# Kernel tuning notes

Measured on AMD Instinct MI355X. Metric: run time of the kernel, lower is better.

Reference implementation:

```python
import jax, jax.numpy as jnp
import numpy as np

NUM_HEADS = 12


def get_rel_pos(q_size, k_size, rel_pos):
    # rel_pos: (2*max(q,k)-1, head_dim); sizes match table here so no resize.
    max_rel_dist = int(2 * max(q_size, k_size) - 1)
    if rel_pos.shape[0] != max_rel_dist:
        rel_pos = jax.image.resize(rel_pos, (max_rel_dist, rel_pos.shape[1]), method='linear')
    q_coords = jnp.arange(q_size)[:, None] * max(k_size / q_size, 1.0)
    k_coords = jnp.arange(k_size)[None, :] * max(q_size / k_size, 1.0)
    rel = (q_coords - k_coords + (k_size - 1) * max(q_size / k_size, 1.0)).astype(jnp.int32)
    return rel_pos[rel.reshape(-1)].reshape(q_size, k_size, -1)  # (q, k, head_dim)


def setup_inputs() -> dict:
    key = jax.random.key(0)
    ks = jax.random.split(key, 7)
    B, H, W, C = 8, 32, 32, 768
    head_dim = C // NUM_HEADS
    return {
        'x': jax.random.normal(ks[0], (B, H, W, C), jnp.float32),
        'w_qkv': jax.random.normal(ks[1], (C, 3 * C), jnp.float32) * 0.02,
        'b_qkv': jnp.zeros((3 * C,), jnp.float32),
        'rel_pos_h': jax.random.normal(ks[2], (2 * H - 1, head_dim), jnp.float32) * 0.02,
        'rel_pos_w': jax.random.normal(ks[3], (2 * W - 1, head_dim), jnp.float32) * 0.02,
        'w_proj': jax.random.normal(ks[4], (C, C), jnp.float32) * 0.02,
        'b_proj': jnp.zeros((C,), jnp.float32),
    }


def reference(x, w_qkv, b_qkv, rel_pos_h, rel_pos_w, w_proj, b_proj):
    B, H, W, C = x.shape
    heads = NUM_HEADS
    hd = C // heads
    S = H * W
    qkv = x @ w_qkv + b_qkv                                  # (B,H,W,3C)
    qkv = qkv.reshape(B, S, 3, heads, hd).transpose(2, 0, 3, 1, 4)
    qkv = qkv.reshape(3, B * heads, S, hd)
    q, k, v = qkv[0], qkv[1], qkv[2]
    attn = (q * hd ** -0.5) @ k.transpose(0, 2, 1)           # (B*heads, S, S)
    rh = get_rel_pos(H, H, rel_pos_h)                        # (H,H,hd)
    rw = get_rel_pos(W, W, rel_pos_w)                        # (W,W,hd)
    r_q = q.reshape(B * heads, H, W, hd)
    rel_h = jnp.einsum('bhwc,hkc->bhwk', r_q, rh)
    rel_w = jnp.einsum('bhwc,wkc->bhwk', r_q, rw)
    attn = (attn.reshape(B * heads, H, W, H, W)
            + rel_h[:, :, :, :, None]
            + rel_w[:, :, :, None, :]).reshape(B * heads, S, S)
    attn = jax.nn.softmax(attn, axis=-1)
    out = (attn @ v).reshape(B, heads, H, W, hd).transpose(0, 2, 3, 1, 4).reshape(B, H, W, C)
    return out @ w_proj + b_proj
```

## Files before the change

### kernel.cpp

```cpp
#include <hip/hip_runtime.h>
#include <hip/hip_bf16.h>

#define BATCH 8
#define SEQ   1024
#define CH    768
#define NH    12
#define HD    64
#define BH    96
#define N_QKV 2304

#define LOG2E 1.44269504088896f

typedef __attribute__((ext_vector_type(8))) short bfrag;
typedef __attribute__((ext_vector_type(4))) short short4v;
typedef __attribute__((ext_vector_type(4))) float ffrag;

__device__ __forceinline__ short f2bf(float x) {
    __hip_bfloat16 h = __float2bfloat16(x);
    return *reinterpret_cast<short*>(&h);
}
__device__ __forceinline__ float bf2f(short b) {
    __hip_bfloat16 h;
    *reinterpret_cast<short*>(&h) = b;
    return __bfloat162float(h);
}
__device__ __forceinline__ void split2(float x, short& hi, short& lo) {
    short h = f2bf(x);
    hi = h;
    lo = f2bf(x - bf2f(h));
}
__device__ __forceinline__ void async_copy16(void* lds, const void* g) {
    __builtin_amdgcn_global_load_lds(
        (const __attribute__((address_space(1))) void*)g,
        (__attribute__((address_space(3))) void*)lds, 16, 0, 0);
}

__global__ __launch_bounds__(256) void prep(
    const float* __restrict__ x,
    const float* __restrict__ w_qkv, const float* __restrict__ w_proj,
    short* __restrict__ Xh,
    short* __restrict__ WqhT, short* __restrict__ WqlT,
    short* __restrict__ WphT, short* __restrict__ WplT)
{
    __shared__ float ts[32][33];
    const int tid = threadIdx.x;
    const int bid = blockIdx.x;

    if (bid < 512) {
        const int n4 = (BATCH * SEQ * CH) / 4;
        for (int i = bid * 256 + tid; i < n4; i += 512 * 256) {
            float4 f = ((const float4*)x)[i];
            short4v h;
            h[0] = f2bf(f.x); h[1] = f2bf(f.y); h[2] = f2bf(f.z); h[3] = f2bf(f.w);
            ((short4v*)Xh)[i] = h;
        }
        return;
    }
    const float* in; short* hiT; short* loT; int R, C, bx, by;
    if (bid < 2240) {
        int t = bid - 512;  bx = t % 72; by = t / 72;
        in = w_qkv; hiT = WqhT; loT = WqlT; R = CH; C = N_QKV;
    } else {
        int t = bid - 2240; bx = t % 24; by = t / 24;
        in = w_proj; hiT = WphT; loT = WplT; R = CH; C = CH;
    }
    const int r0 = by * 32, c0 = bx * 32;
    #pragma unroll
    for (int i = 0; i < 4; ++i) {
        int idx = tid + i * 256;
        int rr = idx >> 5, cc = idx & 31;
        ts[rr][cc] = in[(size_t)(r0 + rr) * C + c0 + cc];
    }
    __syncthreads();
    #pragma unroll
    for (int i = 0; i < 4; ++i) {
        int idx = tid + i * 256;
        int rr = idx >> 5, cc = idx & 31;
        short h, l;
        split2(ts[cc][rr], h, l);
        hiT[(size_t)(c0 + rr) * R + r0 + cc] = h;
        loT[(size_t)(c0 + rr) * R + r0 + cc] = l;
    }
}

__device__ __forceinline__ void gemm_core2(
    short* lds,
    const short* __restrict__ Ah,
    const short* __restrict__ BhT, const short* __restrict__ BlT,
    int m0, int n0, ffrag acc[4][4])
{
    const int tid = threadIdx.x;
    const int wave = tid >> 6, lane = tid & 63;
    const int quad = lane >> 4, l16 = lane & 15;
    const int wm = (wave & 1) * 64, wn = (wave >> 1) * 64;

    const short* src = Ah;
    int row0 = m0, ldso = 0;
    if (wave == 2)      { src = BhT; row0 = n0; ldso = 8192;  }
    else if (wave == 3) { src = BlT; row0 = n0; ldso = 16384; }
    const size_t lane_off = (size_t)(lane >> 3) * CH + (size_t)((lane & 7) ^ (lane >> 3)) * 8;
    const short* sbase = src + (size_t)row0 * CH + lane_off;
    short* ldsw = lds + ldso;

    for (int c = 0; c < 12; ++c) {
        __syncthreads();
        if (wave != 1) {
            #pragma unroll
            for (int i = 0; i < 16; ++i)
                async_copy16(ldsw + i * 512, sbase + (size_t)i * 8 * CH + c * 64);
        }
        __syncthreads();

        #pragma unroll
        for (int kc = 0; kc < 2; ++kc) {
            bfrag ah[4], bh[4], bl[4];
            const int xs = ((kc * 4 + quad) ^ (l16 & 7)) * 8;
            #pragma unroll
            for (int i = 0; i < 4; ++i) {
                int ra = (wm + i * 16 + l16) * 64 + xs;
                int rb = (wn + i * 16 + l16) * 64 + xs;
                ah[i] = *(const bfrag*)&lds[ra];
                bh[i] = *(const bfrag*)&lds[8192 + rb];
                bl[i] = *(const bfrag*)&lds[16384 + rb];
            }
            #pragma unroll
            for (int mi = 0; mi < 4; ++mi)
                #pragma unroll
                for (int ni = 0; ni < 4; ++ni) {
                    acc[mi][ni] = __builtin_amdgcn_mfma_f32_16x16x32_bf16(ah[mi], bh[ni], acc[mi][ni], 0, 0, 0);
                    acc[mi][ni] = __builtin_amdgcn_mfma_f32_16x16x32_bf16(ah[mi], bl[ni], acc[mi][ni], 0, 0, 0);
                }
        }
    }
}

__device__ __forceinline__ void gemm_core3(
    short* lds,
    const short* __restrict__ Ah, const short* __restrict__ Al,
    const short* __restrict__ BhT, const short* __restrict__ BlT,
    int m0, int n0, ffrag acc[4][4])
{
    const int tid = threadIdx.x;
    const int wave = tid >> 6, lane = tid & 63;
    const int quad = lane >> 4, l16 = lane & 15;
    const int wm = (wave & 1) * 64, wn = (wave >> 1) * 64;

    const short* src;
    int row0;
    if (wave == 0)      { src = Ah;  row0 = m0; }
    else if (wave == 1) { src = Al;  row0 = m0; }
    else if (wave == 2) { src = BhT; row0 = n0; }
    else                { src = BlT; row0 = n0; }
    const size_t lane_off = (size_t)(lane >> 3) * CH + (size_t)((lane & 7) ^ (lane >> 3)) * 8;
    const short* sbase = src + (size_t)row0 * CH + lane_off;
    short* ldsw = lds + wave * 8192;

    for (int c = 0; c < 12; ++c) {
        __syncthreads();
        #pragma unroll
        for (int i = 0; i < 16; ++i)
            async_copy16(ldsw + i * 512, sbase + (size_t)i * 8 * CH + c * 64);
        __syncthreads();

        #pragma unroll
        for (int kc = 0; kc < 2; ++kc) {
            bfrag ah[4], al[4], bh[4], bl[4];
            const int xs = ((kc * 4 + quad) ^ (l16 & 7)) * 8;
            #pragma unroll
            for (int i = 0; i < 4; ++i) {
                int ra = (wm + i * 16 + l16) * 64 + xs;
                int rb = (wn + i * 16 + l16) * 64 + xs;
                ah[i] = *(const bfrag*)&lds[ra];
                al[i] = *(const bfrag*)&lds[8192 + ra];
                bh[i] = *(const bfrag*)&lds[16384 + rb];
                bl[i] = *(const bfrag*)&lds[24576 + rb];
            }
            #pragma unroll
            for (int mi = 0; mi < 4; ++mi)
                #pragma unroll
                for (int ni = 0; ni < 4; ++ni) {
                    acc[mi][ni] = __builtin_amdgcn_mfma_f32_16x16x32_bf16(ah[mi], bh[ni], acc[mi][ni], 0, 0, 0);
                    acc[mi][ni] = __builtin_amdgcn_mfma_f32_16x16x32_bf16(ah[mi], bl[ni], acc[mi][ni], 0, 0, 0);
                    acc[mi][ni] = __builtin_amdgcn_mfma_f32_16x16x32_bf16(al[mi], bh[ni], acc[mi][ni], 0, 0, 0);
                }
        }
    }
}

__global__ __launch_bounds__(256) void gemm_qkv_mfma(
    const short* __restrict__ Xh,
    const short* __restrict__ WhT, const short* __restrict__ WlT,
    const float* __restrict__ bias,
    short* __restrict__ qh, short* __restrict__ kh, short* __restrict__ vT)
{
    __shared__ short lds[3 * 8192];
    const int id  = blockIdx.x;
    const int xcd = id & 7;
    const int per = id >> 3;
    const int m0 = (xcd * 8 + per / 18) * 128;
    const int n0 = (per % 18) * 128;
    const int which = n0 / CH;

    ffrag acc[4][4];
    #pragma unroll
    for (int i = 0; i < 4; ++i)
        #pragma unroll
        for (int j = 0; j < 4; ++j) acc[i][j] = (ffrag){0.f, 0.f, 0.f, 0.f};

    gemm_core2(lds, Xh, WhT, WlT, m0, n0, acc);

    const int tid = threadIdx.x;
    const int wave = tid >> 6, lane = tid & 63;
    const int quad = lane >> 4, l16 = lane & 15;
    const int wm = (wave & 1) * 64, wn = (wave >> 1) * 64;
    const int b = m0 >> 10;

    #pragma unroll
    for (int ni = 0; ni < 4; ++ni) {
        int n = n0 + wn + ni * 16 + l16;
        float bv = bias[n];
        int nin = n - which * CH;
        int head = nin >> 6, d = nin & 63;
        #pragma unroll
        for (int mi = 0; mi < 4; ++mi) {
            if (which == 2) {
                int s_base = (m0 & 1023) + wm + mi * 16 + quad * 4;
                short4v pk;
                #pragma unroll
                for (int r = 0; r < 4; ++r) pk[r] = f2bf(acc[mi][ni][r] + bv);
                *(short4v*)&vT[((size_t)(b * NH + head) * HD + d) * SEQ + s_base] = pk;
            } else {
                const float scale = (which == 0) ? 0.125f * LOG2E : 1.0f;
                short* dst = (which == 0) ? qh : kh;
                #pragma unroll
                for (int r = 0; r < 4; ++r) {
                    int m = m0 + wm + mi * 16 + quad * 4 + r;
                    int s = m & 1023;
                    dst[((size_t)(b * NH + head) * SEQ + s) * HD + d] =
                        f2bf((acc[mi][ni][r] + bv) * scale);
                }
            }
        }
    }
}

__global__ __launch_bounds__(256) void gemm_proj_mfma(
    const short* __restrict__ Ah, const short* __restrict__ Al,
    const short* __restrict__ WhT, const short* __restrict__ WlT,
    const float* __restrict__ bias, float* __restrict__ out)
{
    __shared__ short lds[4 * 8192];
    const int id  = blockIdx.x;
    const int xcd = id & 7;
    const int per = id >> 3;
    const int m0 = (xcd * 8 + per / 6) * 128;
    const int n0 = (per % 6) * 128;

    ffrag acc[4][4];
    #pragma unroll
    for (int i = 0; i < 4; ++i)
        #pragma unroll
        for (int j = 0; j < 4; ++j) acc[i][j] = (ffrag){0.f, 0.f, 0.f, 0.f};

    gemm_core3(lds, Ah, Al, WhT, WlT, m0, n0, acc);

    const int tid = threadIdx.x;
    const int wave = tid >> 6, lane = tid & 63;
    const int quad = lane >> 4, l16 = lane & 15;
    const int wm = (wave & 1) * 64, wn = (wave >> 1) * 64;

    #pragma unroll
    for (int ni = 0; ni < 4; ++ni) {
        int n = n0 + wn + ni * 16 + l16;
        float bv = bias[n];
        #pragma unroll
        for (int mi = 0; mi < 4; ++mi)
            #pragma unroll
            for (int r = 0; r < 4; ++r) {
                int m = m0 + wm + mi * 16 + quad * 4 + r;
                out[(size_t)m * CH + n] = acc[mi][ni][r] + bv;
            }
    }
}

__global__ __launch_bounds__(256, 3) void attn_kernel(
    const short* __restrict__ qh,
    const short* __restrict__ kh_g, const short* __restrict__ vT_g,
    const float* __restrict__ rph,
    const float* __restrict__ rpw,
    short* __restrict__ aoh, short* __restrict__ aol)
{
    const int fid   = blockIdx.x;
    const int xcd   = fid & 7;
    const int inner = fid >> 3;
    const int s0    = (inner & 7) * 128;
    const int bh    = xcd * 12 + (inner >> 3);

    const int tid  = threadIdx.x;
    const int wave = tid >> 6;
    const int lane = tid & 63;
    const int quad = lane >> 4;
    const int l16  = lane & 15;

    __shared__ short Kh[64 * 64];
    __shared__ short Vth[64 * 64];
    __shared__ short Th[128][68];
    __shared__ short Tw_Ps[128 * 68];

    bfrag qfh[2][2];
    #pragma unroll
    for (int g = 0; g < 2; ++g) {
        const size_t qrow = ((size_t)bh * SEQ + s0 + wave * 32 + g * 16 + l16) * HD;
        #pragma unroll
        for (int kc = 0; kc < 2; ++kc)
            qfh[g][kc] = *(const bfrag*)(qh + qrow + kc * 32 + quad * 8);
    }

    #pragma unroll
    for (int table = 0; table < 2; ++table) {
        const float* tbl = table ? rpw : rph;
        #pragma unroll
        for (int n0r = 0; n0r < 64; n0r += 16) {
            int r = n0r + l16;
            bfrag bfr[2];
            #pragma unroll
            for (int kc = 0; kc < 2; ++kc) {
                if (r < 63) {
                    const float* trow = tbl + (size_t)r * HD + kc * 32 + quad * 8;
                    float4 f0 = *(const float4*)(trow);
                    float4 f1 = *(const float4*)(trow + 4);
                    float xs[8] = {f0.x, f0.y, f0.z, f0.w, f1.x, f1.y, f1.z, f1.w};
                    #pragma unroll
                    for (int j = 0; j < 8; ++j) bfr[kc][j] = f2bf(xs[j]);
                } else {
                    #pragma unroll
                    for (int j = 0; j < 8; ++j) bfr[kc][j] = 0;
                }
            }
            #pragma unroll
            for (int g = 0; g < 2; ++g) {
                ffrag acc = {0.f, 0.f, 0.f, 0.f};
                acc = __builtin_amdgcn_mfma_f32_16x16x32_bf16(qfh[g][0], bfr[0], acc, 0, 0, 0);
                acc = __builtin_amdgcn_mfma_f32_16x16x32_bf16(qfh[g][1], bfr[1], acc, 0, 0, 0);
                int row = wave * 32 + g * 16 + quad * 4;
                #pragma unroll
                for (int reg = 0; reg < 4; ++reg) {
                    short v = f2bf(acc[reg] * 8.0f);
                    if (table) Tw_Ps[(row + reg) * 68 + n0r + l16] = v;
                    else       Th[row + reg][n0r + l16] = v;
                }
            }
        }
    }

    int hq_r[2][4];
    float tw_r[2][2][4];
    #pragma unroll
    for (int g = 0; g < 2; ++g)
        #pragma unroll
        for (int reg = 0; reg < 4; ++reg) {
            int qloc = wave * 32 + g * 16 + quad * 4 + reg;
            int s_ = s0 + qloc;
            hq_r[g][reg] = s_ >> 5;
            int wq = s_ & 31;
            tw_r[g][0][reg] = bf2f(Tw_Ps[qloc * 68 + (wq - l16 + 31)]);
            tw_r[g][1][reg] = bf2f(Tw_Ps[qloc * 68 + (wq - 16 - l16 + 31)]);
        }

    float l_part[2][4] = {};
    ffrag Ot[2][4];
    #pragma unroll
    for (int g = 0; g < 2; ++g)
        #pragma unroll
        for (int t = 0; t < 4; ++t) Ot[g][t] = (ffrag){0.f, 0.f, 0.f, 0.f};

    const size_t bh_koff = (size_t)bh * SEQ * HD;
    const size_t bh_voff = (size_t)bh * HD * SEQ;
    const size_t klane = (size_t)(lane >> 3) * HD + (size_t)((lane & 7) ^ (lane >> 3)) * 8;
    const size_t vlane = (size_t)(lane >> 3) * SEQ + (size_t)((lane & 7) ^ (lane >> 3)) * 8;

    for (int c = 0; c < 16; ++c) {
        __syncthreads();
        #pragma unroll
        for (int j = 0; j < 2; ++j) {
            int i = wave * 2 + j;
            async_copy16(Kh + i * 512,
                         kh_g + bh_koff + (size_t)(c * 64 + i * 8) * HD + klane);
            async_copy16(Vth + i * 512,
                         vT_g + bh_voff + (size_t)(i * 8) * SEQ + c * 64 + vlane);
        }
        __syncthreads();

        float th_r[2][2][4];
        #pragma unroll
        for (int g = 0; g < 2; ++g)
            #pragma unroll
            for (int reg = 0; reg < 4; ++reg) {
                int qloc = wave * 32 + g * 16 + quad * 4 + reg;
                th_r[g][0][reg] = bf2f(Th[qloc][hq_r[g][reg] - 2 * c + 31]);
                th_r[g][1][reg] = bf2f(Th[qloc][hq_r[g][reg] - 2 * c - 1 + 31]);
            }

        #pragma unroll
        for (int kt = 0; kt < 4; ++kt) {
            bfrag kbh[2];
            #pragma unroll
            for (int kc = 0; kc < 2; ++kc) {
                int xs = ((kc * 4 + quad) ^ (l16 & 7)) * 8;
                kbh[kc] = *(const bfrag*)&Kh[(kt * 16 + l16) * 64 + xs];
            }
            const int hp = kt >> 1, wp = kt & 1;
            #pragma unroll
            for (int g = 0; g < 2; ++g) {
                ffrag acc = {0.f, 0.f, 0.f, 0.f};
                acc = __builtin_amdgcn_mfma_f32_16x16x32_bf16(qfh[g][0], kbh[0], acc, 0, 0, 0);
                acc = __builtin_amdgcn_mfma_f32_16x16x32_bf16(qfh[g][1], kbh[1], acc, 0, 0, 0);
                int row = wave * 32 + g * 16 + quad * 4;
                #pragma unroll
                for (int reg = 0; reg < 4; ++reg) {
                    float p = exp2f(acc[reg] + th_r[g][hp][reg] + tw_r[g][wp][reg]);
                    l_part[g][reg] += p;
                    Tw_Ps[(row + reg) * 68 + kt * 16 + l16] = f2bf(p);
                }
            }
        }

        bfrag pf[2][2];
        #pragma unroll
        for (int g = 0; g < 2; ++g)
            #pragma unroll
            for (int kc = 0; kc < 2; ++kc)
                pf[g][kc] = *(const bfrag*)&Tw_Ps[(wave * 32 + g * 16 + l16) * 68 + kc * 32 + quad * 8];

        #pragma unroll
        for (int t = 0; t < 4; ++t) {
            int d = t * 16 + l16;
            int x0 = ((0 + quad) ^ (l16 & 7)) * 8;
            int x1 = ((4 + quad) ^ (l16 & 7)) * 8;
            bfrag vh0 = *(const bfrag*)&Vth[d * 64 + x0];
            bfrag vh1 = *(const bfrag*)&Vth[d * 64 + x1];
            #pragma unroll
            for (int g = 0; g < 2; ++g) {
                Ot[g][t] = __builtin_amdgcn_mfma_f32_16x16x32_bf16(pf[g][0], vh0, Ot[g][t], 0, 0, 0);
                Ot[g][t] = __builtin_amdgcn_mfma_f32_16x16x32_bf16(pf[g][1], vh1, Ot[g][t], 0, 0, 0);
            }
        }
    }

    {
        int b = bh / NH, head = bh % NH;
        #pragma unroll
        for (int g = 0; g < 2; ++g) {
            float inv[4];
            #pragma unroll
            for (int reg = 0; reg < 4; ++reg) {
                float r = l_part[g][reg];
                #pragma unroll
                for (int off = 1; off < 16; off <<= 1) r += __shfl_xor(r, off, 16);
                inv[reg] = 1.f / r;
            }
            #pragma unroll
            for (int t = 0; t < 4; ++t) {
                #pragma unroll
                for (int reg = 0; reg < 4; ++reg) {
                    int s_ = s0 + wave * 32 + g * 16 + quad * 4 + reg;
                    int d = t * 16 + l16;
                    size_t idx = ((size_t)(b * SEQ + s_)) * CH + head * HD + d;
                    short h, l;
                    split2(Ot[g][t][reg] * inv[reg], h, l);
                    aoh[idx] = h;
                    aol[idx] = l;
                }
            }
        }
    }
}

extern "C" void kernel_launch(void* const* d_in, const int* in_sizes, int n_in,
                              void* d_out, int out_size, void* d_ws, size_t ws_size,
                              hipStream_t stream) {
    const float* x       = (const float*)d_in[0];
    const float* w_qkv   = (const float*)d_in[1];
    const float* b_qkv   = (const float*)d_in[2];
    const float* rph     = (const float*)d_in[3];
    const float* rpw     = (const float*)d_in[4];
    const float* w_proj  = (const float*)d_in[5];
    const float* b_proj  = (const float*)d_in[6];
    float* out = (float*)d_out;

    const size_t NTOK = (size_t)BATCH * SEQ;
    const size_t XSZ  = NTOK * CH;
    const size_t WQSZ = (size_t)N_QKV * CH;
    const size_t WPSZ = (size_t)CH * CH;
    short* Xh   = (short*)d_ws;
    short* AoL  = Xh + XSZ;
    short* WqhT = AoL + XSZ;
    short* WqlT = WqhT + WQSZ;
    short* WphT = WqlT + WQSZ;
    short* WplT = WphT + WPSZ;
    short* qh = WplT + WPSZ;
    short* kh = qh + XSZ;
    short* vT = kh + XSZ;
    short* aoh = Xh;
    short* aol = AoL;

    prep<<<dim3(2816), 256, 0, stream>>>(x, w_qkv, w_proj,
                                         Xh, WqhT, WqlT, WphT, WplT);
    gemm_qkv_mfma<<<dim3(1152), 256, 0, stream>>>(Xh, WqhT, WqlT, b_qkv,
                                                  qh, kh, vT);
    attn_kernel<<<dim3(768), 256, 0, stream>>>(qh, kh, vT,
                                               rph, rpw, aoh, aol);
    gemm_proj_mfma<<<dim3(384), 256, 0, stream>>>(aoh, aol, WphT, WplT,
                                                  b_proj, out);
}
```

Before: 248.5 us.

## Drop low-bf16 weight split in QKV GEMM and transpose attention score MFMA

```diff
diff --git a/kernel.cpp b/kernel.cpp
--- a/kernel.cpp
+++ b/kernel.cpp
@@ -39,7 +39,7 @@
     const float* __restrict__ x,
     const float* __restrict__ w_qkv, const float* __restrict__ w_proj,
     short* __restrict__ Xh,
-    short* __restrict__ WqhT, short* __restrict__ WqlT,
+    short* __restrict__ WqhT,
     short* __restrict__ WphT, short* __restrict__ WplT)
 {
     __shared__ float ts[32][33];
@@ -56,37 +56,51 @@
         }
         return;
     }
-    const float* in; short* hiT; short* loT; int R, C, bx, by;
     if (bid < 2240) {
-        int t = bid - 512;  bx = t % 72; by = t / 72;
-        in = w_qkv; hiT = WqhT; loT = WqlT; R = CH; C = N_QKV;
-    } else {
-        int t = bid - 2240; bx = t % 24; by = t / 24;
-        in = w_proj; hiT = WphT; loT = WplT; R = CH; C = CH;
-    }
-    const int r0 = by * 32, c0 = bx * 32;
-    #pragma unroll
-    for (int i = 0; i < 4; ++i) {
-        int idx = tid + i * 256;
-        int rr = idx >> 5, cc = idx & 31;
-        ts[rr][cc] = in[(size_t)(r0 + rr) * C + c0 + cc];
-    }
-    __syncthreads();
-    #pragma unroll
-    for (int i = 0; i < 4; ++i) {
-        int idx = tid + i * 256;
-        int rr = idx >> 5, cc = idx & 31;
-        short h, l;
-        split2(ts[cc][rr], h, l);
-        hiT[(size_t)(c0 + rr) * R + r0 + cc] = h;
-        loT[(size_t)(c0 + rr) * R + r0 + cc] = l;
-    }
-}
-
-__device__ __forceinline__ void gemm_core2(
+        int t = bid - 512;
+        const int bx = t % 72, by = t / 72;
+        const int r0 = by * 32, c0 = bx * 32;
+        #pragma unroll
+        for (int i = 0; i < 4; ++i) {
+            int idx = tid + i * 256;
+            int rr = idx >> 5, cc = idx & 31;
+            ts[rr][cc] = w_qkv[(size_t)(r0 + rr) * N_QKV + c0 + cc];
+        }
+        __syncthreads();
+        #pragma unroll
+        for (int i = 0; i < 4; ++i) {
+            int idx = tid + i * 256;
+            int rr = idx >> 5, cc = idx & 31;
+            WqhT[(size_t)(c0 + rr) * CH + r0 + cc] = f2bf(ts[cc][rr]);
+        }
+        return;
+    }
+    {
+        int t = bid - 2240;
+        const int bx = t % 24, by = t / 24;
+        const int r0 = by * 32, c0 = bx * 32;
+        #pragma unroll
+        for (int i = 0; i < 4; ++i) {
+            int idx = tid + i * 256;
+            int rr = idx >> 5, cc = idx & 31;
+            ts[rr][cc] = w_proj[(size_t)(r0 + rr) * CH + c0 + cc];
+        }
+        __syncthreads();
+        #pragma unroll
+        for (int i = 0; i < 4; ++i) {
+            int idx = tid + i * 256;
+            int rr = idx >> 5, cc = idx & 31;
+            short h, l;
+            split2(ts[cc][rr], h, l);
+            WphT[(size_t)(c0 + rr) * CH + r0 + cc] = h;
+            WplT[(size_t)(c0 + rr) * CH + r0 + cc] = l;
+        }
+    }
+}
+
+__device__ __forceinline__ void gemm_core1(
     short* lds,
-    const short* __restrict__ Ah,
-    const short* __restrict__ BhT, const short* __restrict__ BlT,
+    const short* __restrict__ Ah, const short* __restrict__ BhT,
     int m0, int n0, ffrag acc[4][4])
 {
     const int tid = threadIdx.x;
@@ -94,42 +108,35 @@
     const int quad = lane >> 4, l16 = lane & 15;
     const int wm = (wave & 1) * 64, wn = (wave >> 1) * 64;
 
-    const short* src = Ah;
-    int row0 = m0, ldso = 0;
-    if (wave == 2)      { src = BhT; row0 = n0; ldso = 8192;  }
-    else if (wave == 3) { src = BlT; row0 = n0; ldso = 16384; }
+    const int arr  = wave >> 1;
+    const int half = wave & 1;
+    const short* src = arr ? BhT : Ah;
+    const int row0 = (arr ? n0 : m0) + half * 64;
     const size_t lane_off = (size_t)(lane >> 3) * CH + (size_t)((lane & 7) ^ (lane >> 3)) * 8;
     const short* sbase = src + (size_t)row0 * CH + lane_off;
-    short* ldsw = lds + ldso;
+    short* ldsw = lds + arr * 8192 + half * 4096;
 
     for (int c = 0; c < 12; ++c) {
         __syncthreads();
-        if (wave != 1) {
-            #pragma unroll
-            for (int i = 0; i < 16; ++i)
-                async_copy16(ldsw + i * 512, sbase + (size_t)i * 8 * CH + c * 64);
-        }
+        #pragma unroll
+        for (int i = 0; i < 8; ++i)
+            async_copy16(ldsw + i * 512, sbase + (size_t)i * 8 * CH + c * 64);
         __syncthreads();
 
         #pragma unroll
         for (int kc = 0; kc < 2; ++kc) {
-            bfrag ah[4], bh[4], bl[4];
+            bfrag ah[4], bh[4];
             const int xs = ((kc * 4 + quad) ^ (l16 & 7)) * 8;
             #pragma unroll
             for (int i = 0; i < 4; ++i) {
-                int ra = (wm + i * 16 + l16) * 64 + xs;
-                int rb = (wn + i * 16 + l16) * 64 + xs;
-                ah[i] = *(const bfrag*)&lds[ra];
-                bh[i] = *(const bfrag*)&lds[8192 + rb];
-                bl[i] = *(const bfrag*)&lds[16384 + rb];
+                ah[i] = *(const bfrag*)&lds[(wm + i * 16 + l16) * 64 + xs];
+                bh[i] = *(const bfrag*)&lds[8192 + (wn + i * 16 + l16) * 64 + xs];
             }
             #pragma unroll
             for (int mi = 0; mi < 4; ++mi)
                 #pragma unroll
-                for (int ni = 0; ni < 4; ++ni) {
+                for (int ni = 0; ni < 4; ++ni)
                     acc[mi][ni] = __builtin_amdgcn_mfma_f32_16x16x32_bf16(ah[mi], bh[ni], acc[mi][ni], 0, 0, 0);
-                    acc[mi][ni] = __builtin_amdgcn_mfma_f32_16x16x32_bf16(ah[mi], bl[ni], acc[mi][ni], 0, 0, 0);
-                }
         }
     }
 }
@@ -189,11 +196,11 @@
 
 __global__ __launch_bounds__(256) void gemm_qkv_mfma(
     const short* __restrict__ Xh,
-    const short* __restrict__ WhT, const short* __restrict__ WlT,
+    const short* __restrict__ WhT,
     const float* __restrict__ bias,
     short* __restrict__ qh, short* __restrict__ kh, short* __restrict__ vT)
 {
-    __shared__ short lds[3 * 8192];
+    __shared__ short lds[2 * 8192];
     const int id  = blockIdx.x;
     const int xcd = id & 7;
     const int per = id >> 3;
@@ -207,7 +214,7 @@
         #pragma unroll
         for (int j = 0; j < 4; ++j) acc[i][j] = (ffrag){0.f, 0.f, 0.f, 0.f};
 
-    gemm_core2(lds, Xh, WhT, WlT, m0, n0, acc);
+    gemm_core1(lds, Xh, WhT, m0, n0, acc);
 
     const int tid = threadIdx.x;
     const int wave = tid >> 6, lane = tid & 63;
@@ -305,7 +312,7 @@
     __shared__ short Kh[64 * 64];
     __shared__ short Vth[64 * 64];
     __shared__ short Th[128][68];
-    __shared__ short Tw_Ps[128 * 68];
+    __shared__ short Tw_Ps[128 * 72];
 
     bfrag qfh[2][2];
     #pragma unroll
@@ -346,28 +353,27 @@
                 #pragma unroll
                 for (int reg = 0; reg < 4; ++reg) {
                     short v = f2bf(acc[reg] * 8.0f);
-                    if (table) Tw_Ps[(row + reg) * 68 + n0r + l16] = v;
+                    if (table) Tw_Ps[(row + reg) * 72 + n0r + l16] = v;
                     else       Th[row + reg][n0r + l16] = v;
                 }
             }
         }
     }
 
-    int hq_r[2][4];
     float tw_r[2][2][4];
     #pragma unroll
-    for (int g = 0; g < 2; ++g)
-        #pragma unroll
-        for (int reg = 0; reg < 4; ++reg) {
-            int qloc = wave * 32 + g * 16 + quad * 4 + reg;
-            int s_ = s0 + qloc;
-            hq_r[g][reg] = s_ >> 5;
-            int wq = s_ & 31;
-            tw_r[g][0][reg] = bf2f(Tw_Ps[qloc * 68 + (wq - l16 + 31)]);
-            tw_r[g][1][reg] = bf2f(Tw_Ps[qloc * 68 + (wq - 16 - l16 + 31)]);
-        }
-
-    float l_part[2][4] = {};
+    for (int g = 0; g < 2; ++g) {
+        int qloc = wave * 32 + g * 16 + l16;
+        int wq = g * 16 + l16;
+        #pragma unroll
+        for (int p = 0; p < 2; ++p)
+            #pragma unroll
+            for (int reg = 0; reg < 4; ++reg)
+                tw_r[g][p][reg] = bf2f(Tw_Ps[qloc * 72 + (wq - (p * 16 + quad * 4 + reg) + 31)]);
+    }
+    const int hq_w = (s0 >> 5) + wave;
+
+    float l_part[2] = {0.f, 0.f};
     ffrag Ot[2][4];
     #pragma unroll
     for (int g = 0; g < 2; ++g)
@@ -391,15 +397,13 @@
         }
         __syncthreads();
 
-        float th_r[2][2][4];
-        #pragma unroll
-        for (int g = 0; g < 2; ++g)
-            #pragma unroll
-            for (int reg = 0; reg < 4; ++reg) {
-                int qloc = wave * 32 + g * 16 + quad * 4 + reg;
-                th_r[g][0][reg] = bf2f(Th[qloc][hq_r[g][reg] - 2 * c + 31]);
-                th_r[g][1][reg] = bf2f(Th[qloc][hq_r[g][reg] - 2 * c - 1 + 31]);
-            }
+        float th_r[2][2];
+        #pragma unroll
+        for (int g = 0; g < 2; ++g) {
+            int qloc = wave * 32 + g * 16 + l16;
+            th_r[g][0] = bf2f(Th[qloc][hq_w - 2 * c + 31]);
+            th_r[g][1] = bf2f(Th[qloc][hq_w - 2 * c - 1 + 31]);
+        }
 
         #pragma unroll
         for (int kt = 0; kt < 4; ++kt) {
@@ -412,16 +416,20 @@
             const int hp = kt >> 1, wp = kt & 1;
             #pragma unroll
             for (int g = 0; g < 2; ++g) {
-                ffrag acc = {0.f, 0.f, 0.f, 0.f};
-                acc = __builtin_amdgcn_mfma_f32_16x16x32_bf16(qfh[g][0], kbh[0], acc, 0, 0, 0);
-                acc = __builtin_amdgcn_mfma_f32_16x16x32_bf16(qfh[g][1], kbh[1], acc, 0, 0, 0);
-                int row = wave * 32 + g * 16 + quad * 4;
+                ffrag acc;
+                #pragma unroll
+                for (int reg = 0; reg < 4; ++reg)
+                    acc[reg] = th_r[g][hp] + tw_r[g][wp][reg];
+                acc = __builtin_amdgcn_mfma_f32_16x16x32_bf16(kbh[0], qfh[g][0], acc, 0, 0, 0);
+                acc = __builtin_amdgcn_mfma_f32_16x16x32_bf16(kbh[1], qfh[g][1], acc, 0, 0, 0);
+                short4v pk;
                 #pragma unroll
                 for (int reg = 0; reg < 4; ++reg) {
-                    float p = exp2f(acc[reg] + th_r[g][hp][reg] + tw_r[g][wp][reg]);
-                    l_part[g][reg] += p;
-                    Tw_Ps[(row + reg) * 68 + kt * 16 + l16] = f2bf(p);
+                    float p = exp2f(acc[reg]);
+                    l_part[g] += p;
+                    pk[reg] = f2bf(p);
                 }
+                *(short4v*)&Tw_Ps[(wave * 32 + g * 16 + l16) * 72 + kt * 16 + quad * 4] = pk;
             }
         }
 
@@ -429,8 +437,8 @@
         #pragma unroll
         for (int g = 0; g < 2; ++g)
             #pragma unroll
-            for (int kc = 0; kc < 2; ++kc)
-                pf[g][kc] = *(const bfrag*)&Tw_Ps[(wave * 32 + g * 16 + l16) * 68 + kc * 32 + quad * 8];
+            for (int kc2 = 0; kc2 < 2; ++kc2)
+                pf[g][kc2] = *(const bfrag*)&Tw_Ps[(wave * 32 + g * 16 + l16) * 72 + kc2 * 32 + quad * 8];
 
         #pragma unroll
         for (int t = 0; t < 4; ++t) {
@@ -451,14 +459,14 @@
         int b = bh / NH, head = bh % NH;
         #pragma unroll
         for (int g = 0; g < 2; ++g) {
+            float r = l_part[g];
+            r += __shfl_xor(r, 16, 64);
+            r += __shfl_xor(r, 32, 64);
+            float invl = 1.f / r;
             float inv[4];
             #pragma unroll
-            for (int reg = 0; reg < 4; ++reg) {
-                float r = l_part[g][reg];
-                #pragma unroll
-                for (int off = 1; off < 16; off <<= 1) r += __shfl_xor(r, off, 16);
-                inv[reg] = 1.f / r;
-            }
+            for (int reg = 0; reg < 4; ++reg)
+                inv[reg] = __shfl(invl, quad * 4 + reg, 16);
             #pragma unroll
             for (int t = 0; t < 4; ++t) {
                 #pragma unroll
@@ -495,8 +503,7 @@
     short* Xh   = (short*)d_ws;
     short* AoL  = Xh + XSZ;
     short* WqhT = AoL + XSZ;
-    short* WqlT = WqhT + WQSZ;
-    short* WphT = WqlT + WQSZ;
+    short* WphT = WqhT + WQSZ;
     short* WplT = WphT + WPSZ;
     short* qh = WplT + WPSZ;
     short* kh = qh + XSZ;
@@ -505,8 +512,8 @@
     short* aol = AoL;
 
     prep<<<dim3(2816), 256, 0, stream>>>(x, w_qkv, w_proj,
-                                         Xh, WqhT, WqlT, WphT, WplT);
-    gemm_qkv_mfma<<<dim3(1152), 256, 0, stream>>>(Xh, WqhT, WqlT, b_qkv,
+                                         Xh, WqhT, WphT, WplT);
+    gemm_qkv_mfma<<<dim3(1152), 256, 0, stream>>>(Xh, WqhT, b_qkv,
                                                   qh, kh, vT);
     attn_kernel<<<dim3(768), 256, 0, stream>>>(qh, kh, vT,
                                                rph, rpw, aoh, aol);
```

New measurement: 231.1 us. 7.0% less time.
